# Kernel optimization log

Measured on AMD Instinct MI355X. Metric: run time of the kernel, lower is better.

Reference implementation:

```python
import jax, jax.numpy as jnp
import numpy as np

POOL_D, POOL_H, POOL_W = 4, 7, 7
SPATIAL_SCALE = 0.25
SAMPLING_RATIO = 2


def setup_inputs() -> dict:
    key = jax.random.key(0)
    k1, k2, k3, k4 = jax.random.split(key, 4)
    N, C, D, H, W = 2, 128, 32, 64, 64
    features = jax.random.normal(k1, (N, C, D, H, W), dtype=jnp.float32)
    R = 256
    inv = 1.0 / SPATIAL_SCALE  # rois live in image coords; features at stride 4
    batch = jax.random.randint(k2, (R,), 0, N).astype(jnp.float32)
    dims = jnp.array([D, H, W], dtype=jnp.float32)
    starts = jax.random.uniform(k3, (R, 3)) * dims * inv * 0.6
    sizes = (0.1 + 0.3 * jax.random.uniform(k4, (R, 3))) * dims * inv
    z1, y1, x1 = starts[:, 0], starts[:, 1], starts[:, 2]
    z2, y2, x2 = z1 + sizes[:, 0], y1 + sizes[:, 1], x1 + sizes[:, 2]
    # roi layout: (batch_idx, x1, y1, z1, x2, y2, z2)
    rois = jnp.stack([batch, x1, y1, z1, x2, y2, z2], axis=1).astype(jnp.float32)
    return {"features": features, "rois": rois}


def _axis(coords, size):
    # classic RoIAlign border handling: outside [-1, size] -> 0 contribution
    valid = (coords >= -1.0) & (coords <= float(size))
    c = jnp.clip(coords, 0.0, float(size) - 1.0)
    lo = jnp.floor(c)
    hi = jnp.minimum(lo + 1.0, float(size) - 1.0)
    w = c - lo  # weight of the hi corner
    return lo.astype(jnp.int32), hi.astype(jnp.int32), w, valid


def roi_align_3d(features, rois):
    N, C, D, H, W = features.shape
    R = rois.shape[0]
    sr = SAMPLING_RATIO
    b = rois[:, 0].astype(jnp.int32)
    x1 = rois[:, 1] * SPATIAL_SCALE
    y1 = rois[:, 2] * SPATIAL_SCALE
    z1 = rois[:, 3] * SPATIAL_SCALE
    x2 = rois[:, 4] * SPATIAL_SCALE
    y2 = rois[:, 5] * SPATIAL_SCALE
    z2 = rois[:, 6] * SPATIAL_SCALE
    rd = jnp.maximum(z2 - z1, 1.0)
    rh = jnp.maximum(y2 - y1, 1.0)
    rw = jnp.maximum(x2 - x1, 1.0)

    def sample_coords(start, extent, P):
        # sampling_ratio sample centers per output bin -> [R, P*sr]
        t = (jnp.arange(P * sr, dtype=jnp.float32) + 0.5) / sr
        return start[:, None] + t[None, :] * (extent / P)[:, None]

    zs = sample_coords(z1, rd, POOL_D)  # [R, SD]
    ys = sample_coords(y1, rh, POOL_H)  # [R, SH]
    xs = sample_coords(x1, rw, POOL_W)  # [R, SW]
    zlo, zhi, wz, vz = _axis(zs, D)
    ylo, yhi, wy, vy = _axis(ys, H)
    xlo, xhi, wx, vx = _axis(xs, W)

    B = b[:, None, None, None]
    Z = lambda a: a[:, :, None, None]
    Y = lambda a: a[:, None, :, None]
    X = lambda a: a[:, None, None, :]

    def g(zi, yi, xi):
        # gather -> [R, SD, SH, SW, C]
        return features[B, :, Z(zi), Y(yi), X(xi)]

    wz1, wy1, wx1 = Z(wz)[..., None], Y(wy)[..., None], X(wx)[..., None]
    wz0, wy0, wx0 = 1.0 - wz1, 1.0 - wy1, 1.0 - wx1
    val = (g(zlo, ylo, xlo) * (wz0 * wy0 * wx0)
           + g(zlo, ylo, xhi) * (wz0 * wy0 * wx1)
           + g(zlo, yhi, xlo) * (wz0 * wy1 * wx0)
           + g(zlo, yhi, xhi) * (wz0 * wy1 * wx1)
           + g(zhi, ylo, xlo) * (wz1 * wy0 * wx0)
           + g(zhi, ylo, xhi) * (wz1 * wy0 * wx1)
           + g(zhi, yhi, xlo) * (wz1 * wy1 * wx0)
           + g(zhi, yhi, xhi) * (wz1 * wy1 * wx1))
    valid = (Z(vz) & Y(vy) & X(vx))[..., None]
    val = jnp.where(valid, val, 0.0)
    # average the sr^3 samples per bin
    val = val.reshape(R, POOL_D, sr, POOL_H, sr, POOL_W, sr, C)
    out = val.mean(axis=(2, 4, 6))  # [R, PD, PH, PW, C]
    return jnp.transpose(out, (0, 4, 1, 2, 3))  # [R, C, PD, PH, PW]


def reference(features, rois):
    return roi_align_3d(features, rois)
```

## Files before the change

kernel.cpp:

```cpp
#include <hip/hip_runtime.h>

constexpr int C_  = 128;
constexpr int D_  = 32;
constexpr int H_  = 64;
constexpr int W_  = 64;
constexpr int PD = 4;
constexpr int PH = 7;
constexpr int PW = 7;
constexpr int SR = 2;
constexpr float SCALE = 0.25f;
constexpr int S_ = D_ * H_ * W_;
constexpr int BINS_PER_ROI = PD * PH * PW;
constexpr int SLAB = PH * PW;

typedef float vf4 __attribute__((ext_vector_type(4)));

__device__ __forceinline__ void axis2(float start, float extent, int P, int p,
                                      int size, int lo[2], int hi[2],
                                      float w[2], bool v[2]) {
    float bin = extent / (float)P;
#pragma unroll
    for (int u = 0; u < 2; ++u) {
        float t = ((float)(p * SR + u) + 0.5f) / (float)SR;
        float coord = start + t * bin;
        v[u] = (coord >= -1.0f) && (coord <= (float)size);
        float cc = fminf(fmaxf(coord, 0.0f), (float)size - 1.0f);
        float fl = floorf(cc);
        lo[u] = (int)fl;
        hi[u] = min(lo[u] + 1, size - 1);
        w[u] = cc - fl;
    }
}

struct AxisW {
    int base;
    float w[4];
};

__device__ __forceinline__ AxisW axis_merge(float start, float extent, int P,
                                            int p, int size) {
    const float bin = extent / (float)P;
    const float t0 = ((float)(p * SR) + 0.5f) / (float)SR;
    const float c0 = start + t0 * bin;
    const float va = (c0 >= -1.0f && c0 <= (float)size) ? 1.0f : 0.0f;
    const float cc0 = fminf(fmaxf(c0, 0.0f), (float)size - 1.0f);
    const float fl0 = floorf(cc0);
    const int lo0 = (int)fl0;
    const int hi0 = min(lo0 + 1, size - 1);
    const float f0 = cc0 - fl0;
    const float a0 = (1.0f - f0) * va;
    const float a1 = f0 * va;
    const float t1 = ((float)(p * SR + 1) + 0.5f) / (float)SR;
    const float c1 = start + t1 * bin;
    const float vb = (c1 >= -1.0f && c1 <= (float)size) ? 1.0f : 0.0f;
    const float cc1 = fminf(fmaxf(c1, 0.0f), (float)size - 1.0f);
    const float fl1 = floorf(cc1);
    const int lo1 = (int)fl1;
    const int hi1 = min(lo1 + 1, size - 1);
    const float f1 = cc1 - fl1;
    const float b0 = (1.0f - f1) * vb;
    const float b1 = f1 * vb;

    const int dh0 = hi0 - lo0;
    const int dl1 = lo1 - lo0;
    const int dh1 = hi1 - lo0;

    float w0 = a0, w1 = 0.f, w2 = 0.f, w3 = 0.f;
    if (dh0 == 0) w0 += a1; else w1 += a1;
    w0 += (dl1 == 0) ? b0 : 0.f;
    w1 += (dl1 == 1) ? b0 : 0.f;
    w2 += (dl1 == 2) ? b0 : 0.f;
    w0 += (dh1 == 0) ? b1 : 0.f;
    w1 += (dh1 == 1) ? b1 : 0.f;
    w2 += (dh1 == 2) ? b1 : 0.f;
    w3 += (dh1 == 3) ? b1 : 0.f;

    AxisW r;
    r.base = lo0;
    r.w[0] = w0; r.w[1] = w1; r.w[2] = w2; r.w[3] = w3;
    return r;
}

__device__ __forceinline__ unsigned int f2bf(float f) {
    unsigned int u = __float_as_uint(f);
    u += 0x7fffu + ((u >> 16) & 1u);
    return u >> 16;
}

__global__ __launch_bounds__(512) void transpose_bf16(
    const float* __restrict__ in, unsigned int* __restrict__ outp) {
    __shared__ unsigned int tileu[256][64];
    const int n  = blockIdx.y;
    const int s0 = blockIdx.x * 256;
    const int t  = threadIdx.x;

    const float* src = in + (size_t)n * C_ * S_;
    unsigned int* dst = outp + (size_t)n * (C_ / 2) * S_;

    if (n == 0 && blockIdx.x == 0 && t < 256) {
        outp[(size_t)gridDim.y * (C_ / 2) * S_ + t] = 0u;
    }

    {
        const int sl  = t & 63;
        const int cp0 = t >> 6;
#pragma unroll
        for (int p = 0; p < 8; ++p) {
            const int cp = cp0 + 8 * p;
            const int c = cp * 2;
            const vf4 a = __builtin_nontemporal_load(
                (const vf4*)&src[(size_t)c * S_ + (s0 + 4 * sl)]);
            const vf4 b = __builtin_nontemporal_load(
                (const vf4*)&src[(size_t)(c + 1) * S_ + (s0 + 4 * sl)]);
            const int col = cp ^ (sl & 31);
            tileu[4 * sl + 0][col] = f2bf(a.x) | (f2bf(b.x) << 16);
            tileu[4 * sl + 1][col] = f2bf(a.y) | (f2bf(b.y) << 16);
            tileu[4 * sl + 2][col] = f2bf(a.z) | (f2bf(b.z) << 16);
            tileu[4 * sl + 3][col] = f2bf(a.w) | (f2bf(b.w) << 16);
        }
    }
    __syncthreads();
    {
        const int cp2   = (t & 31) * 2;
        const int rbase = t >> 5;
#pragma unroll
        for (int it = 0; it < 16; ++it) {
            const int s = rbase + 16 * it;
            const int w = (s >> 2) & 31;
            uint2 v;
            v.x = tileu[s][cp2 ^ w];
            v.y = tileu[s][(cp2 + 1) ^ w];
            *(uint2*)&dst[(size_t)(s0 + s) * (C_ / 2) + cp2] = v;
        }
    }
}

__global__ __launch_bounds__(512) void roi_align_slot(
    const unsigned short* __restrict__ ft,
    const float* __restrict__ rois,
    float* __restrict__ out,
    int R) {
    __shared__ float tile[8][128];

    int roi, pd, part;
    {
        const int B = blockIdx.x;
        if ((R & 7) == 0) {
            const int xcd = B & 7;
            const int j = B >> 3;
            roi = xcd + 8 * (j / 28);
            const int sub = j % 28;
            pd = sub / 7;
            part = sub - pd * 7;
        } else {
            roi = B / 28;
            const int sub = B - roi * 28;
            pd = sub / 7;
            part = sub - pd * 7;
        }
    }

    const int t = threadIdx.x;
    const int w = t >> 6;
    const int lane = t & 63;
    const int slot = part * 8 + w;

    const float* roip = rois + (size_t)roi * 7;
    const int b = (int)roip[0];
    const float x1 = roip[1] * SCALE, y1 = roip[2] * SCALE, z1 = roip[3] * SCALE;
    const float x2 = roip[4] * SCALE, y2 = roip[5] * SCALE, z2 = roip[6] * SCALE;
    const float rd = fmaxf(z2 - z1, 1.0f);
    const float rh = fmaxf(y2 - y1, 1.0f);
    const float rw = fmaxf(x2 - x1, 1.0f);

    AxisW az = axis_merge(z1, rd, PD, pd, D_);
    {
        const float s = 1.0f / (SR * SR * SR);
        az.w[0] *= s; az.w[1] *= s; az.w[2] *= s; az.w[3] *= s;
    }

    if (slot < SLAB) {
        const int ph = slot / PW;
        const int pw = slot - ph * PW;

        const AxisW ay = axis_merge(y1, rh, PH, ph, H_);
        const AxisW ax = axis_merge(x1, rw, PW, pw, W_);

        const int v = lane >> 4;
        float wxl = ax.w[0];
        wxl = (v == 1) ? ax.w[1] : wxl;
        wxl = (v == 2) ? ax.w[2] : wxl;
        wxl = (v == 3) ? ax.w[3] : wxl;

        float acc[8];
#pragma unroll
        for (int j = 0; j < 8; ++j) acc[j] = 0.f;

        const unsigned short* lanep = ft + (unsigned)lane * 8;

#pragma unroll
        for (int iz = 0; iz < 4; ++iz) {
            const int zz = min(az.base + iz, D_ - 1);
            const unsigned zrow = ((unsigned)b * D_ + (unsigned)zz) * H_;
            const float wzv = az.w[iz];
#pragma unroll
            for (int iy = 0; iy < 4; ++iy) {
                const int yy = min(ay.base + iy, H_ - 1);
                const float wf = (wzv * ay.w[iy]) * wxl;
                const unsigned rowe =
                    ((zrow + (unsigned)yy) * W_ + (unsigned)ax.base) * C_;
                const uint4 q = *(const uint4*)(lanep + rowe);
                acc[0] += wf * __uint_as_float(q.x << 16);
                acc[1] += wf * __uint_as_float(q.x & 0xffff0000u);
                acc[2] += wf * __uint_as_float(q.y << 16);
                acc[3] += wf * __uint_as_float(q.y & 0xffff0000u);
                acc[4] += wf * __uint_as_float(q.z << 16);
                acc[5] += wf * __uint_as_float(q.z & 0xffff0000u);
                acc[6] += wf * __uint_as_float(q.w << 16);
                acc[7] += wf * __uint_as_float(q.w & 0xffff0000u);
            }
        }

#pragma unroll
        for (int j = 0; j < 8; ++j) {
            float s = acc[j];
            s += __shfl_xor(s, 16);
            s += __shfl_xor(s, 32);
            acc[j] = s;
        }
        if (lane < 16) {
#pragma unroll
            for (int j = 0; j < 8; ++j) tile[w][lane * 8 + j] = acc[j];
        }
    }

    __syncthreads();

    const int s0 = part * 8;
    const int nslot = SLAB - s0;
    const size_t obase =
        (size_t)roi * C_ * BINS_PER_ROI + (size_t)pd * SLAB + s0;
    if (nslot >= 8) {
#pragma unroll
        for (int it = 0; it < 2; ++it) {
            const int idx = t + it * 512;
            const int c = idx >> 3;
            const int o = idx & 7;
            __builtin_nontemporal_store(
                tile[o][c], &out[obase + (size_t)c * BINS_PER_ROI + o]);
        }
    } else {
        if (t < C_) {
            __builtin_nontemporal_store(tile[0][t],
                                        &out[obase + (size_t)t * BINS_PER_ROI]);
        }
    }
}

__global__ void roi_align_direct(const float* __restrict__ feat,
                                 const float* __restrict__ rois,
                                 float* __restrict__ out, int total) {
    const int tid = blockIdx.x * blockDim.x + threadIdx.x;
    if (tid >= total) return;
    int t = tid;
    const int pw = t % PW; t /= PW;
    const int ph = t % PH; t /= PH;
    const int pd = t % PD; t /= PD;
    const int c = t % C_;  t /= C_;
    const int r = t;

    const float* roi = rois + (size_t)r * 7;
    const int b = (int)roi[0];
    const float x1 = roi[1] * SCALE, y1 = roi[2] * SCALE, z1 = roi[3] * SCALE;
    const float x2 = roi[4] * SCALE, y2 = roi[5] * SCALE, z2 = roi[6] * SCALE;
    const float rd = fmaxf(z2 - z1, 1.0f);
    const float rh = fmaxf(y2 - y1, 1.0f);
    const float rw = fmaxf(x2 - x1, 1.0f);

    int zlo[2], zhi[2], ylo[2], yhi[2], xlo[2], xhi[2];
    float wz[2], wy[2], wx[2];
    bool vz[2], vy[2], vx[2];
    axis2(z1, rd, PD, pd, D_, zlo, zhi, wz, vz);
    axis2(y1, rh, PH, ph, H_, ylo, yhi, wy, vy);
    axis2(x1, rw, PW, pw, W_, xlo, xhi, wx, vx);

    const float* fc = feat + ((size_t)b * C_ + c) * S_;
    float acc = 0.0f;
#pragma unroll
    for (int i = 0; i < 2; ++i) {
        if (!vz[i]) continue;
#pragma unroll
        for (int j = 0; j < 2; ++j) {
            if (!vy[j]) continue;
            const size_t r00 = ((size_t)zlo[i] * H_ + ylo[j]) * W_;
            const size_t r10 = ((size_t)zhi[i] * H_ + ylo[j]) * W_;
            const size_t r01 = ((size_t)zlo[i] * H_ + yhi[j]) * W_;
            const size_t r11 = ((size_t)zhi[i] * H_ + yhi[j]) * W_;
            const float wz1 = wz[i], wz0 = 1.0f - wz1;
            const float wy1 = wy[j], wy0 = 1.0f - wy1;
#pragma unroll
            for (int k = 0; k < 2; ++k) {
                if (!vx[k]) continue;
                const float wx1 = wx[k], wx0 = 1.0f - wx1;
                acc += wz0 * (wy0 * (wx0 * fc[r00 + xlo[k]] + wx1 * fc[r00 + xhi[k]]) +
                              wy1 * (wx0 * fc[r01 + xlo[k]] + wx1 * fc[r01 + xhi[k]])) +
                       wz1 * (wy0 * (wx0 * fc[r10 + xlo[k]] + wx1 * fc[r10 + xhi[k]]) +
                              wy1 * (wx0 * fc[r11 + xlo[k]] + wx1 * fc[r11 + xhi[k]]));
            }
        }
    }
    out[tid] = acc * (1.0f / (SR * SR * SR));
}

extern "C" void kernel_launch(void* const* d_in, const int* in_sizes, int n_in,
                              void* d_out, int out_size, void* d_ws,
                              size_t ws_size, hipStream_t stream) {
    const float* features = (const float*)d_in[0];
    const float* rois = (const float*)d_in[1];
    float* out = (float*)d_out;

    const int R = in_sizes[1] / 7;
    const int N = in_sizes[0] / (C_ * S_);
    const size_t need = (size_t)in_sizes[0] * sizeof(unsigned short) + 1024;

    if (ws_size >= need) {
        unsigned short* ft = (unsigned short*)d_ws;

        dim3 tg(S_ / 256, N);
        transpose_bf16<<<tg, 512, 0, stream>>>(features, (unsigned int*)ft);

        roi_align_slot<<<R * PD * 7, 512, 0, stream>>>(ft, rois, out, R);
    } else {
        const int total = R * C_ * BINS_PER_ROI;
        roi_align_direct<<<(total + 255) / 256, 256, 0, stream>>>(
            features, rois, out, total);
    }
}
```

Before: 254.1 us.

## Remap RoI slot kernel to 7 waves, batch loads, use packed FMA

Changes the slot kernel from 8 waves to 7 waves per block so the 49 (ph,pw) slots of a depth slice split exactly across 7 blocks, which removes the idle wave and the tail-case store path. All 16 bf16 row loads are issued up front, behind a scheduling barrier, so more memory requests are in flight at once. Accumulation uses 2-wide packed FMAs, and any row whose weight is zero across the whole wave is skipped. Holding 16 uint4 values at once raises register pressure, and the per-element division by 7 in the store loop adds a little integer work.

```diff
diff --git a/kernel.cpp b/kernel.cpp
--- a/kernel.cpp
+++ b/kernel.cpp
@@ -14,6 +14,7 @@
 constexpr int SLAB = PH * PW;
 
 typedef float vf4 __attribute__((ext_vector_type(4)));
+typedef float f32x2 __attribute__((ext_vector_type(2)));
 
 __device__ __forceinline__ void axis2(float start, float extent, int P, int p,
                                       int size, int lo[2], int hi[2],
@@ -135,12 +136,12 @@
     }
 }
 
-__global__ __launch_bounds__(512) void roi_align_slot(
+__global__ __launch_bounds__(448) void roi_align_slot(
     const unsigned short* __restrict__ ft,
     const float* __restrict__ rois,
     float* __restrict__ out,
     int R) {
-    __shared__ float tile[8][128];
+    __shared__ float tile[7][128];
 
     int roi, pd, part;
     {
@@ -163,7 +164,7 @@
     const int t = threadIdx.x;
     const int w = t >> 6;
     const int lane = t & 63;
-    const int slot = part * 8 + w;
+    const int slot = part * 7 + w;
 
     const float* roip = rois + (size_t)roi * 7;
     const int b = (int)roip[0];
@@ -179,81 +180,89 @@
         az.w[0] *= s; az.w[1] *= s; az.w[2] *= s; az.w[3] *= s;
     }
 
-    if (slot < SLAB) {
-        const int ph = slot / PW;
-        const int pw = slot - ph * PW;
-
-        const AxisW ay = axis_merge(y1, rh, PH, ph, H_);
-        const AxisW ax = axis_merge(x1, rw, PW, pw, W_);
-
-        const int v = lane >> 4;
-        float wxl = ax.w[0];
-        wxl = (v == 1) ? ax.w[1] : wxl;
-        wxl = (v == 2) ? ax.w[2] : wxl;
-        wxl = (v == 3) ? ax.w[3] : wxl;
-
-        float acc[8];
-#pragma unroll
-        for (int j = 0; j < 8; ++j) acc[j] = 0.f;
-
-        const unsigned short* lanep = ft + (unsigned)lane * 8;
-
-#pragma unroll
-        for (int iz = 0; iz < 4; ++iz) {
-            const int zz = min(az.base + iz, D_ - 1);
-            const unsigned zrow = ((unsigned)b * D_ + (unsigned)zz) * H_;
-            const float wzv = az.w[iz];
-#pragma unroll
-            for (int iy = 0; iy < 4; ++iy) {
-                const int yy = min(ay.base + iy, H_ - 1);
-                const float wf = (wzv * ay.w[iy]) * wxl;
-                const unsigned rowe =
-                    ((zrow + (unsigned)yy) * W_ + (unsigned)ax.base) * C_;
-                const uint4 q = *(const uint4*)(lanep + rowe);
-                acc[0] += wf * __uint_as_float(q.x << 16);
-                acc[1] += wf * __uint_as_float(q.x & 0xffff0000u);
-                acc[2] += wf * __uint_as_float(q.y << 16);
-                acc[3] += wf * __uint_as_float(q.y & 0xffff0000u);
-                acc[4] += wf * __uint_as_float(q.z << 16);
-                acc[5] += wf * __uint_as_float(q.z & 0xffff0000u);
-                acc[6] += wf * __uint_as_float(q.w << 16);
-                acc[7] += wf * __uint_as_float(q.w & 0xffff0000u);
-            }
-        }
-
-#pragma unroll
-        for (int j = 0; j < 8; ++j) {
-            float s = acc[j];
-            s += __shfl_xor(s, 16);
-            s += __shfl_xor(s, 32);
-            acc[j] = s;
-        }
+    const int ph = slot / PW;
+    const int pw = slot - ph * PW;
+    const AxisW ay = axis_merge(y1, rh, PH, ph, H_);
+    const AxisW ax = axis_merge(x1, rw, PW, pw, W_);
+
+    const int v = lane >> 4;
+    float wxl = ax.w[0];
+    wxl = (v == 1) ? ax.w[1] : wxl;
+    wxl = (v == 2) ? ax.w[2] : wxl;
+    wxl = (v == 3) ? ax.w[3] : wxl;
+
+    const unsigned short* lanep = ft + (unsigned)lane * 8;
+    uint4 q[16];
+#pragma unroll
+    for (int iz = 0; iz < 4; ++iz) {
+        const int zz = min(az.base + iz, D_ - 1);
+        const unsigned zrow = ((unsigned)b * D_ + (unsigned)zz) * H_;
+#pragma unroll
+        for (int iy = 0; iy < 4; ++iy) {
+            const int yy = min(ay.base + iy, H_ - 1);
+            const unsigned rowe =
+                ((zrow + (unsigned)yy) * W_ + (unsigned)ax.base) * C_;
+            q[iz * 4 + iy] = *(const uint4*)(lanep + rowe);
+        }
+    }
+    __builtin_amdgcn_sched_barrier(0);
+
+    f32x2 acc2[4];
+#pragma unroll
+    for (int j = 0; j < 4; ++j) { acc2[j].x = 0.f; acc2[j].y = 0.f; }
+
+#pragma unroll
+    for (int iz = 0; iz < 4; ++iz) {
+        if (__builtin_amdgcn_readfirstlane(
+                (int)__float_as_uint(az.w[iz])) == 0) continue;
+#pragma unroll
+        for (int iy = 0; iy < 4; ++iy) {
+            if (__builtin_amdgcn_readfirstlane(
+                    (int)__float_as_uint(ay.w[iy])) == 0) continue;
+            const float wf = (az.w[iz] * ay.w[iy]) * wxl;
+            f32x2 wf2; wf2.x = wf; wf2.y = wf;
+            const uint4 qq = q[iz * 4 + iy];
+            f32x2 p;
+            p.x = __uint_as_float(qq.x << 16);
+            p.y = __uint_as_float(qq.x & 0xffff0000u);
+            acc2[0] = __builtin_elementwise_fma(p, wf2, acc2[0]);
+            p.x = __uint_as_float(qq.y << 16);
+            p.y = __uint_as_float(qq.y & 0xffff0000u);
+            acc2[1] = __builtin_elementwise_fma(p, wf2, acc2[1]);
+            p.x = __uint_as_float(qq.z << 16);
+            p.y = __uint_as_float(qq.z & 0xffff0000u);
+            acc2[2] = __builtin_elementwise_fma(p, wf2, acc2[2]);
+            p.x = __uint_as_float(qq.w << 16);
+            p.y = __uint_as_float(qq.w & 0xffff0000u);
+            acc2[3] = __builtin_elementwise_fma(p, wf2, acc2[3]);
+        }
+    }
+
+#pragma unroll
+    for (int j = 0; j < 4; ++j) {
+        float sx = acc2[j].x;
+        sx += __shfl_xor(sx, 16);
+        sx += __shfl_xor(sx, 32);
+        float sy = acc2[j].y;
+        sy += __shfl_xor(sy, 16);
+        sy += __shfl_xor(sy, 32);
         if (lane < 16) {
-#pragma unroll
-            for (int j = 0; j < 8; ++j) tile[w][lane * 8 + j] = acc[j];
+            tile[w][lane * 8 + 2 * j]     = sx;
+            tile[w][lane * 8 + 2 * j + 1] = sy;
         }
     }
 
     __syncthreads();
 
-    const int s0 = part * 8;
-    const int nslot = SLAB - s0;
     const size_t obase =
-        (size_t)roi * C_ * BINS_PER_ROI + (size_t)pd * SLAB + s0;
-    if (nslot >= 8) {
-#pragma unroll
-        for (int it = 0; it < 2; ++it) {
-            const int idx = t + it * 512;
-            const int c = idx >> 3;
-            const int o = idx & 7;
-            __builtin_nontemporal_store(
-                tile[o][c], &out[obase + (size_t)c * BINS_PER_ROI + o]);
-        }
-    } else {
-        if (t < C_) {
-            __builtin_nontemporal_store(tile[0][t],
-                                        &out[obase + (size_t)t * BINS_PER_ROI]);
-        }
+        (size_t)roi * C_ * BINS_PER_ROI + (size_t)pd * SLAB + (size_t)part * 7;
+#pragma unroll
+    for (int it = 0; it < 2; ++it) {
+        const int idx = t + it * 448;
+        const int c = idx / 7;
+        const int o = idx - c * 7;
+        __builtin_nontemporal_store(tile[o][c],
+                                    &out[obase + (size_t)c * BINS_PER_ROI + o]);
     }
 }
 
@@ -329,7 +338,7 @@
         dim3 tg(S_ / 256, N);
         transpose_bf16<<<tg, 512, 0, stream>>>(features, (unsigned int*)ft);
 
-        roi_align_slot<<<R * PD * 7, 512, 0, stream>>>(ft, rois, out, R);
+        roi_align_slot<<<R * PD * 7, 448, 0, stream>>>(ft, rois, out, R);
     } else {
         const int total = R * C_ * BINS_PER_ROI;
         roi_align_direct<<<(total + 255) / 256, 256, 0, stream>>>(
```

After: 256.9 us. Within noise of the previous version (+1.1%).
